# Optimization experiments

Measured on AMD Instinct MI355X. Metric: run time of the kernel, lower is better.

Reference implementation:

```python
import jax, jax.numpy as jnp
import numpy as np

FEAT = 128
NCLS = 2
EPS = 1e-5


def setup_inputs() -> dict:
    key = jax.random.key(0)
    k1, k2, k3, k4 = jax.random.split(key, 4)
    probe_x = jax.random.normal(k1, (256, FEAT), dtype=jnp.float32)
    gallery_x = jax.random.normal(k2, (1024, FEAT), dtype=jnp.float32)
    # BatchNorm1d params (init: weight=1, bias=0) + running stats (inference mode)
    bn_weight = jnp.ones((FEAT,), dtype=jnp.float32)
    bn_bias = jnp.zeros((FEAT,), dtype=jnp.float32)
    bn_mean = 0.1 * jax.random.normal(k3, (FEAT,), dtype=jnp.float32)
    bn_var = jnp.abs(jax.random.normal(k4, (FEAT,), dtype=jnp.float32)) + 1.0
    # Linear: weight ~ N(0, 0.001), bias = 0
    W = 0.001 * jax.random.normal(jax.random.fold_in(key, 7), (NCLS, FEAT), dtype=jnp.float32)
    b = jnp.zeros((NCLS,), dtype=jnp.float32)
    return {"probe_x": probe_x, "gallery_x": gallery_x,
            "bn_weight": bn_weight, "bn_bias": bn_bias,
            "bn_mean": bn_mean, "bn_var": bn_var, "W": W, "b": b}


def reference(probe_x, gallery_x, bn_weight, bn_bias, bn_mean, bn_var, W, b):
    # pairwise squared diff: [Np, Ng, F]
    diff = (probe_x[:, None, :] - gallery_x[None, :, :]) ** 2
    # BatchNorm1d (inference: running stats), fused scale/shift per feature
    inv = bn_weight * jax.lax.rsqrt(bn_var + EPS)
    diff = (diff - bn_mean) * inv + bn_bias
    # Linear classifier: [Np, Ng, C]
    cls_encode = jnp.einsum('pgf,cf->pgc', diff, W) + b
    return cls_encode
```

## Files before the change

### kernel.cpp

```cpp
#include <hip/hip_runtime.h>

#define FEAT 128
#define NP   256
#define NG   1024
#define PT   16
#define GT   16
#define LDP  132
#define EPSB 1e-5f

__global__ __launch_bounds__(256) void CLASSIFIER_69956427317336_kernel(
    const float* __restrict__ px,
    const float* __restrict__ gx,
    const float* __restrict__ bw,
    const float* __restrict__ bb,
    const float* __restrict__ bm,
    const float* __restrict__ bv,
    const float* __restrict__ Wm,
    const float* __restrict__ bias,
    float* __restrict__ out)
{
    __shared__ float xs[PT][LDP];
    __shared__ float ys[GT][LDP];
    __shared__ float V0[FEAT];
    __shared__ float V1[FEAT];
    __shared__ float kpart[4];
    __shared__ float Ksh[2];

    const int tid  = threadIdx.x;
    const int p0   = blockIdx.x * PT;
    const int g0   = blockIdx.y * GT;

    {
        int t = tid;
        #pragma unroll
        for (int it = 0; it < 2; ++it, t += 256) {
            const int row = t >> 5;
            const int c4  = t & 31;
            float4 xv = *(const float4*)(px + (size_t)(p0 + row) * FEAT + c4 * 4);
            *(float4*)&xs[row][c4 * 4] = xv;
            float4 yv = *(const float4*)(gx + (size_t)(g0 + row) * FEAT + c4 * 4);
            *(float4*)&ys[row][c4 * 4] = yv;
        }
    }

    {
        const int w    = tid >> 6;
        const int lane = tid & 63;
        const int c    = w & 1;
        const int f    = lane + ((w >> 1) << 6);
        const float inv = bw[f] * rsqrtf(bv[f] + EPSB);
        const float wv  = Wm[c * FEAT + f];
        const float v   = inv * wv;
        if (c == 0) V0[f] = v; else V1[f] = v;
        float kcf = (bb[f] - bm[f] * inv) * wv;
        #pragma unroll
        for (int off = 32; off > 0; off >>= 1) kcf += __shfl_down(kcf, off);
        if (lane == 0) kpart[w] = kcf;
    }
    __syncthreads();
    if (tid < 2) Ksh[tid] = bias[tid] + kpart[tid] + kpart[tid + 2];
    __syncthreads();

    const int gi = tid & (GT - 1);
    const int pi = tid >> 4;

    float acc0 = 0.f, acc1 = 0.f;
    #pragma unroll
    for (int f4 = 0; f4 < FEAT; f4 += 4) {
        const float4 xv = *(const float4*)&xs[pi][f4];
        const float4 yv = *(const float4*)&ys[gi][f4];
        const float4 v0 = *(const float4*)&V0[f4];
        const float4 v1 = *(const float4*)&V1[f4];
        float d, s;
        d = xv.x - yv.x; s = d * d;
        acc0 = fmaf(s, v0.x, acc0); acc1 = fmaf(s, v1.x, acc1);
        d = xv.y - yv.y; s = d * d;
        acc0 = fmaf(s, v0.y, acc0); acc1 = fmaf(s, v1.y, acc1);
        d = xv.z - yv.z; s = d * d;
        acc0 = fmaf(s, v0.z, acc0); acc1 = fmaf(s, v1.z, acc1);
        d = xv.w - yv.w; s = d * d;
        acc0 = fmaf(s, v0.w, acc0); acc1 = fmaf(s, v1.w, acc1);
    }

    const size_t o = ((size_t)(p0 + pi) * NG + (size_t)(g0 + gi)) * 2;
    *(float2*)(out + o) = make_float2(acc0 + Ksh[0], acc1 + Ksh[1]);
}

extern "C" void kernel_launch(void* const* d_in, const int* in_sizes, int n_in,
                              void* d_out, int out_size, void* d_ws, size_t ws_size,
                              hipStream_t stream) {
    const float* px = (const float*)d_in[0];
    const float* gx = (const float*)d_in[1];
    const float* bw = (const float*)d_in[2];
    const float* bb = (const float*)d_in[3];
    const float* bm = (const float*)d_in[4];
    const float* bv = (const float*)d_in[5];
    const float* Wm = (const float*)d_in[6];
    const float* bs = (const float*)d_in[7];
    float* out = (float*)d_out;

    dim3 grid(NP / PT, NG / GT);
    dim3 block(256);
    CLASSIFIER_69956427317336_kernel<<<grid, block, 0, stream>>>(
        px, gx, bw, bb, bm, bv, Wm, bs, out);
}
```

Measured before the change: 12.77 us.

## Expand squared difference into GEMM-like form with precomputed norms and larger g-tile

```diff
diff --git a/kernel.cpp b/kernel.cpp
--- a/kernel.cpp
+++ b/kernel.cpp
@@ -4,9 +4,35 @@
 #define NP   256
 #define NG   1024
 #define PT   16
-#define GT   16
+#define GT   32
 #define LDP  132
 #define EPSB 1e-5f
+
+#define FMA4(acc, xv, vv) \
+    acc = fmaf((xv).x, (vv).x, acc); \
+    acc = fmaf((xv).y, (vv).y, acc); \
+    acc = fmaf((xv).z, (vv).z, acc); \
+    acc = fmaf((xv).w, (vv).w, acc);
+
+__device__ __forceinline__ void yv_one(const float4 y, const float4 v0, const float4 v1,
+                                       float4& z0, float4& z1, float& b0, float& b1) {
+    z0.x = -2.f * y.x * v0.x; z1.x = -2.f * y.x * v1.x;
+    b0 = fmaf(y.x * y.x, v0.x, b0); b1 = fmaf(y.x * y.x, v1.x, b1);
+    z0.y = -2.f * y.y * v0.y; z1.y = -2.f * y.y * v1.y;
+    b0 = fmaf(y.y * y.y, v0.y, b0); b1 = fmaf(y.y * y.y, v1.y, b1);
+    z0.z = -2.f * y.z * v0.z; z1.z = -2.f * y.z * v1.z;
+    b0 = fmaf(y.z * y.z, v0.z, b0); b1 = fmaf(y.z * y.z, v1.z, b1);
+    z0.w = -2.f * y.w * v0.w; z1.w = -2.f * y.w * v1.w;
+    b0 = fmaf(y.w * y.w, v0.w, b0); b1 = fmaf(y.w * y.w, v1.w, b1);
+}
+
+__device__ __forceinline__ void a_one(const float4 x, const float4 v0, const float4 v1,
+                                      float& a0, float& a1) {
+    a0 = fmaf(x.x * x.x, v0.x, a0); a1 = fmaf(x.x * x.x, v1.x, a1);
+    a0 = fmaf(x.y * x.y, v0.y, a0); a1 = fmaf(x.y * x.y, v1.y, a1);
+    a0 = fmaf(x.z * x.z, v0.z, a0); a1 = fmaf(x.z * x.z, v1.z, a1);
+    a0 = fmaf(x.w * x.w, v0.w, a0); a1 = fmaf(x.w * x.w, v1.w, a1);
+}
 
 __global__ __launch_bounds__(256) void CLASSIFIER_69956427317336_kernel(
     const float* __restrict__ px,
@@ -19,76 +45,115 @@
     const float* __restrict__ bias,
     float* __restrict__ out)
 {
-    __shared__ float xs[PT][LDP];
-    __shared__ float ys[GT][LDP];
-    __shared__ float V0[FEAT];
-    __shared__ float V1[FEAT];
+    __shared__ __align__(16) float xs[PT][LDP];
+    __shared__ __align__(16) float yv0s[GT][LDP];
+    __shared__ __align__(16) float yv1s[GT][LDP];
+    __shared__ __align__(16) float V0[FEAT];
+    __shared__ __align__(16) float V1[FEAT];
+    __shared__ float Ash[PT][2];
+    __shared__ float Bsh[GT][2];
     __shared__ float kpart[4];
     __shared__ float Ksh[2];
 
-    const int tid  = threadIdx.x;
-    const int p0   = blockIdx.x * PT;
-    const int g0   = blockIdx.y * GT;
+    const int tid = threadIdx.x;
+    const int p0 = blockIdx.x * PT;
+    const int g0 = blockIdx.y * GT;
+
+    const int gg = tid >> 3, ge = tid & 7;
+    const float4* grow = (const float4*)(gx + (size_t)(g0 + gg) * FEAT);
+    float4 gv0 = grow[ge];
+    float4 gv1 = grow[ge + 8];
+    float4 gv2 = grow[ge + 16];
+    float4 gv3 = grow[ge + 24];
+
+    const int pp = tid >> 4, pe = tid & 15;
+    const float4* prow = (const float4*)(px + (size_t)(p0 + pp) * FEAT);
+    float4 pv0 = prow[pe];
+    float4 pv1 = prow[pe + 16];
 
     {
-        int t = tid;
-        #pragma unroll
-        for (int it = 0; it < 2; ++it, t += 256) {
-            const int row = t >> 5;
-            const int c4  = t & 31;
-            float4 xv = *(const float4*)(px + (size_t)(p0 + row) * FEAT + c4 * 4);
-            *(float4*)&xs[row][c4 * 4] = xv;
-            float4 yv = *(const float4*)(gx + (size_t)(g0 + row) * FEAT + c4 * 4);
-            *(float4*)&ys[row][c4 * 4] = yv;
-        }
-    }
-
-    {
-        const int w    = tid >> 6;
-        const int lane = tid & 63;
-        const int c    = w & 1;
-        const int f    = lane + ((w >> 1) << 6);
+        const int c = tid >> 7, f = tid & 127;
         const float inv = bw[f] * rsqrtf(bv[f] + EPSB);
         const float wv  = Wm[c * FEAT + f];
         const float v   = inv * wv;
         if (c == 0) V0[f] = v; else V1[f] = v;
-        float kcf = (bb[f] - bm[f] * inv) * wv;
+        float kt = (bb[f] - bm[f] * inv) * wv;
         #pragma unroll
-        for (int off = 32; off > 0; off >>= 1) kcf += __shfl_down(kcf, off);
-        if (lane == 0) kpart[w] = kcf;
+        for (int off = 32; off > 0; off >>= 1) kt += __shfl_down(kt, off);
+        if ((tid & 63) == 0) kpart[tid >> 6] = kt;
     }
     __syncthreads();
-    if (tid < 2) Ksh[tid] = bias[tid] + kpart[tid] + kpart[tid + 2];
+    if (tid < 2) Ksh[tid] = bias[tid] + kpart[tid * 2] + kpart[tid * 2 + 1];
+
+    {
+        float b0 = 0.f, b1 = 0.f;
+        float4* w0 = (float4*)&yv0s[gg][0];
+        float4* w1 = (float4*)&yv1s[gg][0];
+        const float4* v0p = (const float4*)V0;
+        const float4* v1p = (const float4*)V1;
+        float4 z0, z1;
+        yv_one(gv0, v0p[ge],      v1p[ge],      z0, z1, b0, b1); w0[ge]      = z0; w1[ge]      = z1;
+        yv_one(gv1, v0p[ge + 8],  v1p[ge + 8],  z0, z1, b0, b1); w0[ge + 8]  = z0; w1[ge + 8]  = z1;
+        yv_one(gv2, v0p[ge + 16], v1p[ge + 16], z0, z1, b0, b1); w0[ge + 16] = z0; w1[ge + 16] = z1;
+        yv_one(gv3, v0p[ge + 24], v1p[ge + 24], z0, z1, b0, b1); w0[ge + 24] = z0; w1[ge + 24] = z1;
+        #pragma unroll
+        for (int off = 4; off > 0; off >>= 1) {
+            b0 += __shfl_down(b0, off, 8);
+            b1 += __shfl_down(b1, off, 8);
+        }
+        if (ge == 0) { Bsh[gg][0] = b0; Bsh[gg][1] = b1; }
+    }
+
+    {
+        float a0 = 0.f, a1 = 0.f;
+        float4* wx = (float4*)&xs[pp][0];
+        const float4* v0p = (const float4*)V0;
+        const float4* v1p = (const float4*)V1;
+        wx[pe]      = pv0;
+        wx[pe + 16] = pv1;
+        a_one(pv0, v0p[pe],      v1p[pe],      a0, a1);
+        a_one(pv1, v0p[pe + 16], v1p[pe + 16], a0, a1);
+        #pragma unroll
+        for (int off = 8; off > 0; off >>= 1) {
+            a0 += __shfl_down(a0, off, 16);
+            a1 += __shfl_down(a1, off, 16);
+        }
+        if (pe == 0) { Ash[pp][0] = a0; Ash[pp][1] = a1; }
+    }
     __syncthreads();
 
-    const int gi = tid & (GT - 1);
-    const int pi = tid >> 4;
+    const int pi = tid >> 4, j = tid & 15;
+    float acc00 = Ash[pi][0] + Bsh[j][0]      + Ksh[0];
+    float acc01 = Ash[pi][1] + Bsh[j][1]      + Ksh[1];
+    float acc10 = Ash[pi][0] + Bsh[j + 16][0] + Ksh[0];
+    float acc11 = Ash[pi][1] + Bsh[j + 16][1] + Ksh[1];
 
-    float acc0 = 0.f, acc1 = 0.f;
-    #pragma unroll
-    for (int f4 = 0; f4 < FEAT; f4 += 4) {
-        const float4 xv = *(const float4*)&xs[pi][f4];
-        const float4 yv = *(const float4*)&ys[gi][f4];
-        const float4 v0 = *(const float4*)&V0[f4];
-        const float4 v1 = *(const float4*)&V1[f4];
-        float d, s;
-        d = xv.x - yv.x; s = d * d;
-        acc0 = fmaf(s, v0.x, acc0); acc1 = fmaf(s, v1.x, acc1);
-        d = xv.y - yv.y; s = d * d;
-        acc0 = fmaf(s, v0.y, acc0); acc1 = fmaf(s, v1.y, acc1);
-        d = xv.z - yv.z; s = d * d;
-        acc0 = fmaf(s, v0.z, acc0); acc1 = fmaf(s, v1.z, acc1);
-        d = xv.w - yv.w; s = d * d;
-        acc0 = fmaf(s, v0.w, acc0); acc1 = fmaf(s, v1.w, acc1);
+    const float4* xr  = (const float4*)&xs[pi][0];
+    const float4* y0a = (const float4*)&yv0s[j][0];
+    const float4* y1a = (const float4*)&yv1s[j][0];
+    const float4* y0b = (const float4*)&yv0s[j + 16][0];
+    const float4* y1b = (const float4*)&yv1s[j + 16][0];
+
+    #pragma unroll 4
+    for (int i = 0; i < FEAT / 4; ++i) {
+        const float4 xv  = xr[i];
+        const float4 a0v = y0a[i], a1v = y1a[i];
+        const float4 b0v = y0b[i], b1v = y1b[i];
+        FMA4(acc00, xv, a0v)
+        FMA4(acc01, xv, a1v)
+        FMA4(acc10, xv, b0v)
+        FMA4(acc11, xv, b1v)
     }
 
-    const size_t o = ((size_t)(p0 + pi) * NG + (size_t)(g0 + gi)) * 2;
-    *(float2*)(out + o) = make_float2(acc0 + Ksh[0], acc1 + Ksh[1]);
+    const size_t ob = ((size_t)(p0 + pi) * NG + (size_t)(g0 + j)) * 2;
+    *(float2*)(out + ob)      = make_float2(acc00, acc01);
+    *(float2*)(out + ob + 32) = make_float2(acc10, acc11);
 }
 
 extern "C" void kernel_launch(void* const* d_in, const int* in_sizes, int n_in,
                               void* d_out, int out_size, void* d_ws, size_t ws_size,
                               hipStream_t stream) {
+    (void)in_sizes; (void)n_in; (void)out_size; (void)d_ws; (void)ws_size;
     const float* px = (const float*)d_in[0];
     const float* gx = (const float*)d_in[1];
     const float* bw = (const float*)d_in[2];
```

After: 13.65 us. 6.9% more time.
